# Performance work log

Hardware: AMD Instinct MI355X
Metric: run time of the kernel (lower is better)

Reference implementation:

```python
import jax, jax.numpy as jnp
import numpy as np

B, K, DIM, T_FRAMES = 4, 200, 256, 800

def _conv1d_same(x, w, b):
    # x: [B, K, Cin], w: [3, Cin, Cout] (WIO), 'same' padding over token axis
    y = jax.lax.conv_general_dilated(x, w, window_strides=(1,), padding='SAME',
                                     dimension_numbers=('NWC', 'WIO', 'NWC'))
    return y + b

def _swish_block(x, w1, b1, w2, b2):
    x = jax.nn.silu(x @ w1 + b1)
    return jax.nn.silu(x @ w2 + b2)

def setup_inputs() -> dict:
    key = jax.random.key(0)
    ks = jax.random.split(key, 10)
    def lin(k, fan_in, shape):
        return jax.random.normal(k, shape, dtype=jnp.float32) / np.sqrt(fan_in)
    inp = {
        'T': T_FRAMES,
        'durations': jax.random.uniform(ks[0], (B, K), dtype=jnp.float32) * 4.0,
        'features': jax.random.normal(ks[1], (B, K, DIM), dtype=jnp.float32),
        'conv1_w': lin(ks[2], 3 * DIM, (3, DIM, 8)),
        'conv1_b': jnp.zeros((8,), jnp.float32),
        'conv2_w': lin(ks[3], 3 * DIM, (3, DIM, 8)),
        'conv2_b': jnp.zeros((8,), jnp.float32),
        'sw1_w1': lin(ks[4], 10, (10, 16)), 'sw1_b1': jnp.zeros((16,), jnp.float32),
        'sw1_w2': lin(ks[5], 16, (16, 16)), 'sw1_b2': jnp.zeros((16,), jnp.float32),
        'sw2_w1': lin(ks[6], 10, (10, 2)), 'sw2_b1': jnp.zeros((2,), jnp.float32),
        'sw2_w2': lin(ks[7], 2, (2, 2)), 'sw2_b2': jnp.zeros((2,), jnp.float32),
        'p1_w': lin(ks[8], 2, (2, 1)), 'p1_b': jnp.zeros((1,), jnp.float32),
        'p2_w': lin(ks[9], 16, (16, DIM)), 'p2_b': jnp.zeros((DIM,), jnp.float32),
    }
    return inp

def reference(T, durations, features, conv1_w, conv1_b, conv2_w, conv2_b,
              sw1_w1, sw1_b1, sw1_w2, sw1_b2, sw2_w1, sw2_b1, sw2_w2, sw2_b2,
              p1_w, p1_b, p2_w, p2_b):
    # Conv + SiLU token feature extraction: [B, K, 8]
    left = jax.nn.silu(_conv1d_same(features, conv1_w, conv1_b))
    right = jax.nn.silu(_conv1d_same(features, conv2_w, conv2_b))
    # Token boundary grids S, E: [B, T, K]
    token_end = jnp.cumsum(durations, axis=1)          # [B, K]
    token_start = token_end - durations                # [B, K]
    t = jnp.arange(T, dtype=features.dtype)            # frame index grid
    S = t[None, :, None] - token_start[:, None, :]     # [B, T, K]
    E = token_end[:, None, :] - t[None, :, None]       # [B, T, K]
    Bn, Tn, Kn = S.shape
    # Concat (S, E, conv_feats) -> [B, T, K, 10]
    xleft = jnp.concatenate([S[..., None], E[..., None],
                             jnp.broadcast_to(left[:, None], (Bn, Tn, Kn, 8))], axis=-1)
    xright = jnp.concatenate([S[..., None], E[..., None],
                              jnp.broadcast_to(right[:, None], (Bn, Tn, Kn, 8))], axis=-1)
    C = _swish_block(xleft, sw1_w1, sw1_b1, sw1_w2, sw1_b2)      # [B, T, K, 16]
    r = _swish_block(xright, sw2_w1, sw2_b1, sw2_w2, sw2_b2)     # [B, T, K, 2]
    logits = (r @ p1_w + p1_b)[..., 0]                           # [B, T, K]
    W = jax.nn.softmax(logits, axis=-1)                          # attention over tokens
    # Upsampled output: weighted token features + projected auxiliary context
    O = jnp.einsum('btk,bkd->btd', W, features)
    A = jnp.einsum('btk,btkp->btp', W, C)                        # [B, T, 16]
    return O + (A @ p2_w + p2_b)
```

## Files before the change

kernel.cpp:

```cpp
#include <hip/hip_runtime.h>
#include <math.h>

#define B_   4
#define K_   200
#define DIM_ 256
#define T_   800

#define S_UP 68

__device__ __forceinline__ float silu_f(float x) {
    return x / (1.0f + __expf(-x));
}

__global__ __launch_bounds__(256) void prep_kernel(
        const float* __restrict__ dur,
        const float* __restrict__ feats,
        const float* __restrict__ c1w, const float* __restrict__ c1b,
        const float* __restrict__ c2w, const float* __restrict__ c2b,
        const float* __restrict__ sw1_w1, const float* __restrict__ sw1_b1,
        const float* __restrict__ sw2_w1, const float* __restrict__ sw2_b1,
        float* __restrict__ cw) {
    const int b = blockIdx.y, k0 = blockIdx.x * 4;
    const int tid = threadIdx.x, w = tid >> 6, l = tid & 63;

    __shared__ float wT[16][772];
    __shared__ float red[64][S_UP];
    __shared__ float sSc[K_], sEc[K_];
    __shared__ float sfeat[4][16];

    for (int i = tid; i < 3 * DIM_ * 8; i += 256) {
        int tc = i >> 3, o = i & 7;
        wT[o][tc]     = c1w[i];
        wT[8 + o][tc] = c2w[i];
    }
    if (tid < 64) {
        float4 dv = make_float4(0.f, 0.f, 0.f, 0.f);
        if (tid < 50) dv = *(const float4*)&dur[b * K_ + tid * 4];
        float s0 = dv.x, s1 = s0 + dv.y, s2 = s1 + dv.z, s3 = s2 + dv.w;
        float sc = s3;
#pragma unroll
        for (int off = 1; off < 64; off <<= 1) {
            float v = __shfl_up(sc, off);
            if (tid >= off) sc += v;
        }
        float excl = sc - s3;
        if (tid < 50) {
            *(float4*)&sSc[tid * 4] = make_float4(excl, excl + s0, excl + s1, excl + s2);
            *(float4*)&sEc[tid * 4] = make_float4(excl + s0, excl + s1, excl + s2, excl + s3);
        }
    }
    __syncthreads();

    {
        const int k = k0 + w;
        const float4* f4 = (const float4*)feats;
        float4 fv[3];
#pragma unroll
        for (int tap = 0; tap < 3; ++tap) {
            int kk = k - 1 + tap;
            bool valid = (kk >= 0 && kk < K_);
            int kc = valid ? kk : 0;
            float4 v = f4[(size_t)(b * K_ + kc) * 64 + l];
            fv[tap] = valid ? v : make_float4(0.f, 0.f, 0.f, 0.f);
        }
        float acc[16];
#pragma unroll
        for (int oc = 0; oc < 16; ++oc) acc[oc] = 0.f;
#pragma unroll
        for (int tap = 0; tap < 3; ++tap) {
#pragma unroll
            for (int oc = 0; oc < 16; ++oc) {
                float4 wv = *(const float4*)&wT[oc][tap * DIM_ + 4 * l];
                acc[oc] += fv[tap].x * wv.x + fv[tap].y * wv.y
                         + fv[tap].z * wv.z + fv[tap].w * wv.w;
            }
        }
#pragma unroll
        for (int oc = 0; oc < 16; ++oc) red[w * 16 + oc][l] = acc[oc];
    }
    __syncthreads();
    {
        const int rwv = tid >> 6, oc = (tid >> 2) & 15, rq = tid & 3;
        const float* base = &red[rwv * 16 + oc][rq * 16];
        float4 b0 = *(const float4*)&base[0];
        float4 b1 = *(const float4*)&base[4];
        float4 b2 = *(const float4*)&base[8];
        float4 b3 = *(const float4*)&base[12];
        float s = b0.x + b0.y + b0.z + b0.w + b1.x + b1.y + b1.z + b1.w
                + b2.x + b2.y + b2.z + b2.w + b3.x + b3.y + b3.z + b3.w;
        s += __shfl_down(s, 1);
        s += __shfl_down(s, 2);
        if (rq == 0) {
            float bias = (oc < 8) ? c1b[oc] : c2b[oc & 7];
            sfeat[rwv][oc] = silu_f(s + bias);
        }
    }
    __syncthreads();

    if (tid < 64) {
        const int j = tid >> 2, klc = tid & 3, kk = k0 + klc;
        float st = sSc[kk], en = sEc[kk];
        float a = sw1_b1[j] - st * sw1_w1[j] + en * sw1_w1[16 + j];
#pragma unroll
        for (int i = 0; i < 8; ++i) a += sfeat[klc][i] * sw1_w1[(2 + i) * 16 + j];
        cw[(b * 18 + 2 + j) * K_ + kk] = a;
    } else if (tid < 72) {
        const int idx = tid - 64, which = idx >> 2, klc = idx & 3, kk = k0 + klc;
        float st = sSc[kk], en = sEc[kk];
        float a = sw2_b1[which] - st * sw2_w1[which] + en * sw2_w1[2 + which];
#pragma unroll
        for (int i = 0; i < 8; ++i) a += sfeat[klc][8 + i] * sw2_w1[(2 + i) * 2 + which];
        cw[(b * 18 + which) * K_ + kk] = a;
    }
}

__global__ __launch_bounds__(256, 3) void main_kernel(
        const float* __restrict__ feats,
        const float* __restrict__ cw,
        const float* __restrict__ sw1_w1, const float* __restrict__ sw1_w2,
        const float* __restrict__ sw1_b2,
        const float* __restrict__ sw2_w1, const float* __restrict__ sw2_w2,
        const float* __restrict__ sw2_b2,
        const float* __restrict__ p1_w,   const float* __restrict__ p1_b,
        const float* __restrict__ p2_w,   const float* __restrict__ p2_b,
        float* __restrict__ out) {
    const int t0 = blockIdx.x * 4, b = blockIdx.y;
    const int tid = threadIdx.x, w = tid >> 6, l = tid & 63;
    const int t = t0 + w;

    __shared__ alignas(16) float upool[128 * S_UP];
    __shared__ alignas(16) float W4[K_][4];
    __shared__ alignas(16) float At[16][4];
    __shared__ float lw2T[16][16];
    __shared__ float lb2s[16];

    lw2T[tid & 15][tid >> 4] = sw1_w2[tid];
    if (tid < 16) lb2s[tid] = sw1_b2[tid];

    const float* cbg = cw + b * 18 * K_;
    int kc[4];
#pragma unroll
    for (int i = 0; i < 4; ++i) { int k = l + 64 * i; kc[i] = (k < K_) ? k : (K_ - 1); }
    float Bv[4][16];
#pragma unroll
    for (int j = 0; j < 16; ++j)
#pragma unroll
        for (int i = 0; i < 4; ++i) Bv[i][j] = cbg[(2 + j) * K_ + kc[i]];
    float c0[4], c1[4];
#pragma unroll
    for (int i = 0; i < 4; ++i) { c0[i] = cbg[kc[i]]; c1[i] = cbg[K_ + kc[i]]; }

    __syncthreads();

    const float tf = (float)t;
    const float a0 = sw2_w1[0] - sw2_w1[2], a1 = sw2_w1[1] - sw2_w1[3];
    const float rw20 = sw2_w2[0], rw21 = sw2_w2[1], rw22 = sw2_w2[2], rw23 = sw2_w2[3];
    const float rb20 = sw2_b2[0], rb21 = sw2_b2[1];
    const float p10 = p1_w[0], p11 = p1_w[1], p1b0 = p1_b[0];

    float lg[4];
#pragma unroll
    for (int i = 0; i < 4; ++i) {
        float h0 = silu_f(fmaf(a0, tf, c0[i]));
        float h1 = silu_f(fmaf(a1, tf, c1[i]));
        float g0 = silu_f(rb20 + h0 * rw20 + h1 * rw22);
        float g1 = silu_f(rb21 + h0 * rw21 + h1 * rw23);
        lg[i] = (l + 64 * i < K_) ? (g0 * p10 + g1 * p11 + p1b0) : -1e30f;
    }
    float m = fmaxf(fmaxf(lg[0], lg[1]), fmaxf(lg[2], lg[3]));
#pragma unroll
    for (int off = 32; off > 0; off >>= 1) m = fmaxf(m, __shfl_xor(m, off));
    float e0 = __expf(lg[0] - m), e1 = __expf(lg[1] - m);
    float e2 = __expf(lg[2] - m), e3 = __expf(lg[3] - m);
    float ssum = e0 + e1 + e2 + e3;
#pragma unroll
    for (int off = 32; off > 0; off >>= 1) ssum += __shfl_xor(ssum, off);
    float inv = 1.0f / ssum;
    float wgt[4] = { e0 * inv, e1 * inv, e2 * inv, e3 * inv };
#pragma unroll
    for (int i = 0; i < 4; ++i) { int k = l + 64 * i; if (k < K_) W4[k][w] = wgt[i]; }

    const int kb = w * 50;
    const float4* fB4 = (const float4*)(feats + (size_t)b * K_ * DIM_);
    float4 pf[8];
#pragma unroll
    for (int q = 0; q < 8; ++q) pf[q] = fB4[(size_t)(kb + q) * 64 + l];

    float ajt[16];
#pragma unroll
    for (int j = 0; j < 16; ++j) ajt[j] = (sw1_w1[j] - sw1_w1[16 + j]) * tf;
    float hmat[4][16];
#pragma unroll
    for (int j = 0; j < 16; ++j)
#pragma unroll
        for (int i = 0; i < 4; ++i) hmat[i][j] = silu_f(ajt[j] + Bv[i][j]);
    float acc[16];
#pragma unroll
    for (int j = 0; j < 16; ++j) {
        float4 w0 = *(const float4*)&lw2T[j][0];
        float4 w1v = *(const float4*)&lw2T[j][4];
        float4 w2v = *(const float4*)&lw2T[j][8];
        float4 w3v = *(const float4*)&lw2T[j][12];
        float bj = lb2s[j];
        float s = 0.f;
#pragma unroll
        for (int i = 0; i < 4; ++i) {
            float c = bj
                + hmat[i][0]  * w0.x  + hmat[i][1]  * w0.y  + hmat[i][2]  * w0.z  + hmat[i][3]  * w0.w
                + hmat[i][4]  * w1v.x + hmat[i][5]  * w1v.y + hmat[i][6]  * w1v.z + hmat[i][7]  * w1v.w
                + hmat[i][8]  * w2v.x + hmat[i][9]  * w2v.y + hmat[i][10] * w2v.z + hmat[i][11] * w2v.w
                + hmat[i][12] * w3v.x + hmat[i][13] * w3v.y + hmat[i][14] * w3v.z + hmat[i][15] * w3v.w;
            s += wgt[i] * silu_f(c);
        }
        acc[j] = s;
    }
#pragma unroll
    for (int j = 0; j < 16; ++j) upool[(w * 16 + j) * S_UP + l] = acc[j];

    __syncthreads();

    {
        const int rwv = tid >> 6, rj = (tid >> 2) & 15, rq = tid & 3;
        const float* base = &upool[(rwv * 16 + rj) * S_UP + rq * 16];
        float4 b0 = *(const float4*)&base[0];
        float4 b1 = *(const float4*)&base[4];
        float4 b2 = *(const float4*)&base[8];
        float4 b3 = *(const float4*)&base[12];
        float s = b0.x + b0.y + b0.z + b0.w + b1.x + b1.y + b1.z + b1.w
                + b2.x + b2.y + b2.z + b2.w + b3.x + b3.y + b3.z + b3.w;
        s += __shfl_down(s, 1);
        s += __shfl_down(s, 2);
        if (rq == 0) At[rj][rwv] = s;
    }

    {
        float4 po[4];
#pragma unroll
        for (int f = 0; f < 4; ++f) po[f] = make_float4(0.f, 0.f, 0.f, 0.f);
#pragma unroll
        for (int kk = 0; kk < 8; ++kk) {
            float4 wv = *(const float4*)&W4[kb + kk][0];
            float4 fv = pf[kk];
            po[0].x += wv.x * fv.x; po[0].y += wv.x * fv.y; po[0].z += wv.x * fv.z; po[0].w += wv.x * fv.w;
            po[1].x += wv.y * fv.x; po[1].y += wv.y * fv.y; po[1].z += wv.y * fv.z; po[1].w += wv.y * fv.w;
            po[2].x += wv.z * fv.x; po[2].y += wv.z * fv.y; po[2].z += wv.z * fv.z; po[2].w += wv.z * fv.w;
            po[3].x += wv.w * fv.x; po[3].y += wv.w * fv.y; po[3].z += wv.w * fv.z; po[3].w += wv.w * fv.w;
        }
#pragma unroll 6
        for (int kk = 8; kk < 50; ++kk) {
            float4 wv = *(const float4*)&W4[kb + kk][0];
            float4 fv = fB4[(size_t)(kb + kk) * 64 + l];
            po[0].x += wv.x * fv.x; po[0].y += wv.x * fv.y; po[0].z += wv.x * fv.z; po[0].w += wv.x * fv.w;
            po[1].x += wv.y * fv.x; po[1].y += wv.y * fv.y; po[1].z += wv.y * fv.z; po[1].w += wv.y * fv.w;
            po[2].x += wv.z * fv.x; po[2].y += wv.z * fv.y; po[2].z += wv.z * fv.z; po[2].w += wv.z * fv.w;
            po[3].x += wv.w * fv.x; po[3].y += wv.w * fv.y; po[3].z += wv.w * fv.z; po[3].w += wv.w * fv.w;
        }
#pragma unroll
        for (int f = 0; f < 4; ++f) {
            upool[(64 + w * 16 + f * 4 + 0) * S_UP + l] = po[f].x;
            upool[(64 + w * 16 + f * 4 + 1) * S_UP + l] = po[f].y;
            upool[(64 + w * 16 + f * 4 + 2) * S_UP + l] = po[f].z;
            upool[(64 + w * 16 + f * 4 + 3) * S_UP + l] = po[f].w;
        }
    }
    __syncthreads();

    {
        const int d = tid, l0 = d >> 2, q = d & 3;
        float v0 = 0.f, v1 = 0.f, v2 = 0.f, v3 = 0.f;
#pragma unroll
        for (int ww = 0; ww < 4; ++ww) {
            v0 += upool[(64 + ww * 16 + 0 * 4 + q) * S_UP + l0];
            v1 += upool[(64 + ww * 16 + 1 * 4 + q) * S_UP + l0];
            v2 += upool[(64 + ww * 16 + 2 * 4 + q) * S_UP + l0];
            v3 += upool[(64 + ww * 16 + 3 * 4 + q) * S_UP + l0];
        }
        float ab = p2_b[d];
        v0 += ab; v1 += ab; v2 += ab; v3 += ab;
#pragma unroll
        for (int p = 0; p < 16; ++p) {
            float pw = p2_w[p * DIM_ + d];
            float4 av = *(const float4*)&At[p][0];
            v0 += av.x * pw; v1 += av.y * pw; v2 += av.z * pw; v3 += av.w * pw;
        }
        float* op = out + ((size_t)b * T_ + t0) * DIM_ + d;
        op[0 * DIM_] = v0;
        op[1 * DIM_] = v1;
        op[2 * DIM_] = v2;
        op[3 * DIM_] = v3;
    }
}

extern "C" void kernel_launch(void* const* d_in, const int* in_sizes, int n_in,
                              void* d_out, int out_size, void* d_ws, size_t ws_size,
                              hipStream_t stream) {
    const float* durations = (const float*)d_in[1];
    const float* features  = (const float*)d_in[2];
    const float* conv1_w   = (const float*)d_in[3];
    const float* conv1_b   = (const float*)d_in[4];
    const float* conv2_w   = (const float*)d_in[5];
    const float* conv2_b   = (const float*)d_in[6];
    const float* sw1_w1    = (const float*)d_in[7];
    const float* sw1_b1    = (const float*)d_in[8];
    const float* sw1_w2    = (const float*)d_in[9];
    const float* sw1_b2    = (const float*)d_in[10];
    const float* sw2_w1    = (const float*)d_in[11];
    const float* sw2_b1    = (const float*)d_in[12];
    const float* sw2_w2    = (const float*)d_in[13];
    const float* sw2_b2    = (const float*)d_in[14];
    const float* p1_w      = (const float*)d_in[15];
    const float* p1_b      = (const float*)d_in[16];
    const float* p2_w      = (const float*)d_in[17];
    const float* p2_b      = (const float*)d_in[18];
    float* out = (float*)d_out;

    float* cw = (float*)d_ws;

    prep_kernel<<<dim3(50, B_), 256, 0, stream>>>(
        durations, features, conv1_w, conv1_b, conv2_w, conv2_b,
        sw1_w1, sw1_b1, sw2_w1, sw2_b1, cw);
    main_kernel<<<dim3(T_ / 4, B_), 256, 0, stream>>>(
        features, cw,
        sw1_w1, sw1_w2, sw1_b2,
        sw2_w1, sw2_w2, sw2_b2,
        p1_w, p1_b, p2_w, p2_b, out);
}
```

Measured before the change: 130.2 us.

## Restructure main kernel to 8 frames per 512-thread block with contiguous token tiles

```diff
diff --git a/kernel.cpp b/kernel.cpp
--- a/kernel.cpp
+++ b/kernel.cpp
@@ -7,9 +7,15 @@
 #define T_   800
 
 #define S_UP 68
+#define S_O  66
+#define KP_  204
 
 __device__ __forceinline__ float silu_f(float x) {
     return x / (1.0f + __expf(-x));
+}
+__device__ __forceinline__ void fma4(float4& a, float s, const float4& v) {
+    a.x = fmaf(s, v.x, a.x); a.y = fmaf(s, v.y, a.y);
+    a.z = fmaf(s, v.z, a.z); a.w = fmaf(s, v.w, a.w);
 }
 
 __global__ __launch_bounds__(256) void prep_kernel(
@@ -114,7 +120,7 @@
     }
 }
 
-__global__ __launch_bounds__(256, 3) void main_kernel(
+__global__ __launch_bounds__(512, 4) void main_kernel(
         const float* __restrict__ feats,
         const float* __restrict__ cw,
         const float* __restrict__ sw1_w1, const float* __restrict__ sw1_w2,
@@ -124,48 +130,48 @@
         const float* __restrict__ p1_w,   const float* __restrict__ p1_b,
         const float* __restrict__ p2_w,   const float* __restrict__ p2_b,
         float* __restrict__ out) {
-    const int t0 = blockIdx.x * 4, b = blockIdx.y;
+    const int t0 = blockIdx.x * 8, b = blockIdx.y;
     const int tid = threadIdx.x, w = tid >> 6, l = tid & 63;
-    const int t = t0 + w;
-
-    __shared__ alignas(16) float upool[128 * S_UP];
-    __shared__ alignas(16) float W4[K_][4];
-    __shared__ alignas(16) float At[16][4];
-    __shared__ float lw2T[16][16];
-    __shared__ float lb2s[16];
-
-    lw2T[tid & 15][tid >> 4] = sw1_w2[tid];
+    const float tf = (float)(t0 + w);
+
+    __shared__ alignas(16) float upool[128 * S_O];
+    __shared__ alignas(16) float W8[8][KP_];
+    __shared__ alignas(16) float At[16][8];
+    __shared__ alignas(16) float lw2R[256];
+    __shared__ alignas(16) float lb2s[16];
+
+    if (tid < 256) lw2R[tid] = sw1_w2[tid];
     if (tid < 16) lb2s[tid] = sw1_b2[tid];
 
+    const int  kbase = (l < 50) ? 4 * l : 196;
+    const bool kv    = (l < 50);
     const float* cbg = cw + b * 18 * K_;
-    int kc[4];
-#pragma unroll
-    for (int i = 0; i < 4; ++i) { int k = l + 64 * i; kc[i] = (k < K_) ? k : (K_ - 1); }
-    float Bv[4][16];
-#pragma unroll
-    for (int j = 0; j < 16; ++j)
-#pragma unroll
-        for (int i = 0; i < 4; ++i) Bv[i][j] = cbg[(2 + j) * K_ + kc[i]];
-    float c0[4], c1[4];
-#pragma unroll
-    for (int i = 0; i < 4; ++i) { c0[i] = cbg[kc[i]]; c1[i] = cbg[K_ + kc[i]]; }
-
-    __syncthreads();
-
-    const float tf = (float)t;
+
+    float4 c0v = *(const float4*)&cbg[kbase];
+    float4 c1v = *(const float4*)&cbg[K_ + kbase];
+    float4 Bcur[4], Bnxt[4];
+#pragma unroll
+    for (int j = 0; j < 4; ++j) Bcur[j] = *(const float4*)&cbg[(2 + j) * K_ + kbase];
+
+    __syncthreads();
+
     const float a0 = sw2_w1[0] - sw2_w1[2], a1 = sw2_w1[1] - sw2_w1[3];
     const float rw20 = sw2_w2[0], rw21 = sw2_w2[1], rw22 = sw2_w2[2], rw23 = sw2_w2[3];
     const float rb20 = sw2_b2[0], rb21 = sw2_b2[1];
     const float p10 = p1_w[0], p11 = p1_w[1], p1b0 = p1_b[0];
 
     float lg[4];
-#pragma unroll
-    for (int i = 0; i < 4; ++i) {
-        float h0 = silu_f(fmaf(a0, tf, c0[i]));
-        float h1 = silu_f(fmaf(a1, tf, c1[i]));
-        float g0 = silu_f(rb20 + h0 * rw20 + h1 * rw22);
-        float g1 = silu_f(rb21 + h0 * rw21 + h1 * rw23);
-        lg[i] = (l + 64 * i < K_) ? (g0 * p10 + g1 * p11 + p1b0) : -1e30f;
+    {
+        float c0a[4] = { c0v.x, c0v.y, c0v.z, c0v.w };
+        float c1a[4] = { c1v.x, c1v.y, c1v.z, c1v.w };
+#pragma unroll
+        for (int i = 0; i < 4; ++i) {
+            float h0 = silu_f(fmaf(a0, tf, c0a[i]));
+            float h1 = silu_f(fmaf(a1, tf, c1a[i]));
+            float g0 = silu_f(rb20 + h0 * rw20 + h1 * rw22);
+            float g1 = silu_f(rb21 + h0 * rw21 + h1 * rw23);
+            lg[i] = kv ? (g0 * p10 + g1 * p11 + p1b0) : -1e30f;
+        }
     }
     float m = fmaxf(fmaxf(lg[0], lg[1]), fmaxf(lg[2], lg[3]));
 #pragma unroll
@@ -177,51 +183,65 @@
     for (int off = 32; off > 0; off >>= 1) ssum += __shfl_xor(ssum, off);
     float inv = 1.0f / ssum;
     float wgt[4] = { e0 * inv, e1 * inv, e2 * inv, e3 * inv };
-#pragma unroll
-    for (int i = 0; i < 4; ++i) { int k = l + 64 * i; if (k < K_) W4[k][w] = wgt[i]; }
-
-    const int kb = w * 50;
+    if (kv) *(float4*)&W8[w][kbase] = make_float4(wgt[0], wgt[1], wgt[2], wgt[3]);
+
+    const int kb = 25 * w;
     const float4* fB4 = (const float4*)(feats + (size_t)b * K_ * DIM_);
-    float4 pf[8];
-#pragma unroll
-    for (int q = 0; q < 8; ++q) pf[q] = fB4[(size_t)(kb + q) * 64 + l];
-
-    float ajt[16];
-#pragma unroll
-    for (int j = 0; j < 16; ++j) ajt[j] = (sw1_w1[j] - sw1_w1[16 + j]) * tf;
-    float hmat[4][16];
-#pragma unroll
-    for (int j = 0; j < 16; ++j)
-#pragma unroll
-        for (int i = 0; i < 4; ++i) hmat[i][j] = silu_f(ajt[j] + Bv[i][j]);
-    float acc[16];
-#pragma unroll
-    for (int j = 0; j < 16; ++j) {
-        float4 w0 = *(const float4*)&lw2T[j][0];
-        float4 w1v = *(const float4*)&lw2T[j][4];
-        float4 w2v = *(const float4*)&lw2T[j][8];
-        float4 w3v = *(const float4*)&lw2T[j][12];
-        float bj = lb2s[j];
-        float s = 0.f;
-#pragma unroll
-        for (int i = 0; i < 4; ++i) {
-            float c = bj
-                + hmat[i][0]  * w0.x  + hmat[i][1]  * w0.y  + hmat[i][2]  * w0.z  + hmat[i][3]  * w0.w
-                + hmat[i][4]  * w1v.x + hmat[i][5]  * w1v.y + hmat[i][6]  * w1v.z + hmat[i][7]  * w1v.w
-                + hmat[i][8]  * w2v.x + hmat[i][9]  * w2v.y + hmat[i][10] * w2v.z + hmat[i][11] * w2v.w
-                + hmat[i][12] * w3v.x + hmat[i][13] * w3v.y + hmat[i][14] * w3v.z + hmat[i][15] * w3v.w;
-            s += wgt[i] * silu_f(c);
-        }
-        acc[j] = s;
-    }
-#pragma unroll
-    for (int j = 0; j < 16; ++j) upool[(w * 16 + j) * S_UP + l] = acc[j];
-
-    __syncthreads();
-
+    float4 pf0 = fB4[(size_t)kb * 64 + l];
+    float4 pf1 = fB4[(size_t)(kb + 1) * 64 + l];
+
+    float4 cacc[4][4];
+#pragma unroll
+    for (int i = 0; i < 4; ++i)
+#pragma unroll
+        for (int q = 0; q < 4; ++q) cacc[i][q] = make_float4(0.f, 0.f, 0.f, 0.f);
+
+#pragma unroll
+    for (int grp = 0; grp < 4; ++grp) {
+        if (grp < 3) {
+#pragma unroll
+            for (int j = 0; j < 4; ++j)
+                Bnxt[j] = *(const float4*)&cbg[(2 + grp * 4 + 4 + j) * K_ + kbase];
+        }
+#pragma unroll
+        for (int j = 0; j < 4; ++j) {
+            const int jj = grp * 4 + j;
+            float aj = (sw1_w1[jj] - sw1_w1[16 + jj]) * tf;
+            float h0 = silu_f(aj + Bcur[j].x);
+            float h1 = silu_f(aj + Bcur[j].y);
+            float h2 = silu_f(aj + Bcur[j].z);
+            float h3 = silu_f(aj + Bcur[j].w);
+#pragma unroll
+            for (int q = 0; q < 4; ++q) {
+                float4 wv = *(const float4*)&lw2R[jj * 16 + 4 * q];
+                fma4(cacc[0][q], h0, wv);
+                fma4(cacc[1][q], h1, wv);
+                fma4(cacc[2][q], h2, wv);
+                fma4(cacc[3][q], h3, wv);
+            }
+        }
+#pragma unroll
+        for (int j = 0; j < 4; ++j) Bcur[j] = Bnxt[j];
+    }
+#pragma unroll
+    for (int q = 0; q < 4; ++q) {
+        float4 bb = *(const float4*)&lb2s[4 * q];
+        float sx = wgt[0] * silu_f(cacc[0][q].x + bb.x) + wgt[1] * silu_f(cacc[1][q].x + bb.x)
+                 + wgt[2] * silu_f(cacc[2][q].x + bb.x) + wgt[3] * silu_f(cacc[3][q].x + bb.x);
+        float sy = wgt[0] * silu_f(cacc[0][q].y + bb.y) + wgt[1] * silu_f(cacc[1][q].y + bb.y)
+                 + wgt[2] * silu_f(cacc[2][q].y + bb.y) + wgt[3] * silu_f(cacc[3][q].y + bb.y);
+        float sz = wgt[0] * silu_f(cacc[0][q].z + bb.z) + wgt[1] * silu_f(cacc[1][q].z + bb.z)
+                 + wgt[2] * silu_f(cacc[2][q].z + bb.z) + wgt[3] * silu_f(cacc[3][q].z + bb.z);
+        float sw = wgt[0] * silu_f(cacc[0][q].w + bb.w) + wgt[1] * silu_f(cacc[1][q].w + bb.w)
+                 + wgt[2] * silu_f(cacc[2][q].w + bb.w) + wgt[3] * silu_f(cacc[3][q].w + bb.w);
+        upool[(w * 16 + 4 * q + 0) * S_O + l] = sx;
+        upool[(w * 16 + 4 * q + 1) * S_O + l] = sy;
+        upool[(w * 16 + 4 * q + 2) * S_O + l] = sz;
+        upool[(w * 16 + 4 * q + 3) * S_O + l] = sw;
+    }
     {
-        const int rwv = tid >> 6, rj = (tid >> 2) & 15, rq = tid & 3;
-        const float* base = &upool[(rwv * 16 + rj) * S_UP + rq * 16];
+        const int rj = (l >> 2) & 15, rq = l & 3;
+        const float* base = &upool[(w * 16 + rj) * S_O + rq * 16];
         float4 b0 = *(const float4*)&base[0];
         float4 b1 = *(const float4*)&base[4];
         float4 b2 = *(const float4*)&base[8];
@@ -230,64 +250,57 @@
                 + b2.x + b2.y + b2.z + b2.w + b3.x + b3.y + b3.z + b3.w;
         s += __shfl_down(s, 1);
         s += __shfl_down(s, 2);
-        if (rq == 0) At[rj][rwv] = s;
-    }
-
-    {
+        if (rq == 0) At[rj][w] = s;
+    }
+    __syncthreads();
+
+    const int d = tid & 255, f0 = tid >> 8;
+    const int l0 = d >> 2, qq = d & 3;
+
+#pragma unroll
+    for (int half = 0; half < 2; ++half) {
         float4 po[4];
 #pragma unroll
         for (int f = 0; f < 4; ++f) po[f] = make_float4(0.f, 0.f, 0.f, 0.f);
-#pragma unroll
-        for (int kk = 0; kk < 8; ++kk) {
-            float4 wv = *(const float4*)&W4[kb + kk][0];
-            float4 fv = pf[kk];
-            po[0].x += wv.x * fv.x; po[0].y += wv.x * fv.y; po[0].z += wv.x * fv.z; po[0].w += wv.x * fv.w;
-            po[1].x += wv.y * fv.x; po[1].y += wv.y * fv.y; po[1].z += wv.y * fv.z; po[1].w += wv.y * fv.w;
-            po[2].x += wv.z * fv.x; po[2].y += wv.z * fv.y; po[2].z += wv.z * fv.z; po[2].w += wv.z * fv.w;
-            po[3].x += wv.w * fv.x; po[3].y += wv.w * fv.y; po[3].z += wv.w * fv.z; po[3].w += wv.w * fv.w;
-        }
-#pragma unroll 6
-        for (int kk = 8; kk < 50; ++kk) {
-            float4 wv = *(const float4*)&W4[kb + kk][0];
-            float4 fv = fB4[(size_t)(kb + kk) * 64 + l];
-            po[0].x += wv.x * fv.x; po[0].y += wv.x * fv.y; po[0].z += wv.x * fv.z; po[0].w += wv.x * fv.w;
-            po[1].x += wv.y * fv.x; po[1].y += wv.y * fv.y; po[1].z += wv.y * fv.z; po[1].w += wv.y * fv.w;
-            po[2].x += wv.z * fv.x; po[2].y += wv.z * fv.y; po[2].z += wv.z * fv.z; po[2].w += wv.z * fv.w;
-            po[3].x += wv.w * fv.x; po[3].y += wv.w * fv.y; po[3].z += wv.w * fv.z; po[3].w += wv.w * fv.w;
+        const float* Wr0 = W8[half * 4 + 0];
+        const float* Wr1 = W8[half * 4 + 1];
+        const float* Wr2 = W8[half * 4 + 2];
+        const float* Wr3 = W8[half * 4 + 3];
+#pragma unroll 5
+        for (int kk = 0; kk < 25; ++kk) {
+            const int k = kb + kk;
+            float4 fv;
+            if (half == 0 && kk == 0)      fv = pf0;
+            else if (half == 0 && kk == 1) fv = pf1;
+            else                           fv = fB4[(size_t)k * 64 + l];
+            float w0 = Wr0[k], w1 = Wr1[k], w2 = Wr2[k], w3 = Wr3[k];
+            fma4(po[0], w0, fv);
+            fma4(po[1], w1, fv);
+            fma4(po[2], w2, fv);
+            fma4(po[3], w3, fv);
         }
 #pragma unroll
         for (int f = 0; f < 4; ++f) {
-            upool[(64 + w * 16 + f * 4 + 0) * S_UP + l] = po[f].x;
-            upool[(64 + w * 16 + f * 4 + 1) * S_UP + l] = po[f].y;
-            upool[(64 + w * 16 + f * 4 + 2) * S_UP + l] = po[f].z;
-            upool[(64 + w * 16 + f * 4 + 3) * S_UP + l] = po[f].w;
-        }
-    }
-    __syncthreads();
-
-    {
-        const int d = tid, l0 = d >> 2, q = d & 3;
-        float v0 = 0.f, v1 = 0.f, v2 = 0.f, v3 = 0.f;
-#pragma unroll
-        for (int ww = 0; ww < 4; ++ww) {
-            v0 += upool[(64 + ww * 16 + 0 * 4 + q) * S_UP + l0];
-            v1 += upool[(64 + ww * 16 + 1 * 4 + q) * S_UP + l0];
-            v2 += upool[(64 + ww * 16 + 2 * 4 + q) * S_UP + l0];
-            v3 += upool[(64 + ww * 16 + 3 * 4 + q) * S_UP + l0];
-        }
-        float ab = p2_b[d];
-        v0 += ab; v1 += ab; v2 += ab; v3 += ab;
-#pragma unroll
-        for (int p = 0; p < 16; ++p) {
-            float pw = p2_w[p * DIM_ + d];
-            float4 av = *(const float4*)&At[p][0];
-            v0 += av.x * pw; v1 += av.y * pw; v2 += av.z * pw; v3 += av.w * pw;
-        }
-        float* op = out + ((size_t)b * T_ + t0) * DIM_ + d;
-        op[0 * DIM_] = v0;
-        op[1 * DIM_] = v1;
-        op[2 * DIM_] = v2;
-        op[3 * DIM_] = v3;
+            upool[(w * 16 + f * 4 + 0) * S_O + l] = po[f].x;
+            upool[(w * 16 + f * 4 + 1) * S_O + l] = po[f].y;
+            upool[(w * 16 + f * 4 + 2) * S_O + l] = po[f].z;
+            upool[(w * 16 + f * 4 + 3) * S_O + l] = po[f].w;
+        }
+        __syncthreads();
+
+#pragma unroll
+        for (int ffi = 0; ffi < 2; ++ffi) {
+            const int fr = f0 + 2 * ffi;
+            float v = p2_b[d];
+#pragma unroll
+            for (int ww = 0; ww < 8; ++ww)
+                v += upool[(ww * 16 + fr * 4 + qq) * S_O + l0];
+#pragma unroll
+            for (int p = 0; p < 16; ++p)
+                v += At[p][half * 4 + fr] * p2_w[p * DIM_ + d];
+            out[((size_t)b * T_ + t0 + half * 4 + fr) * DIM_ + d] = v;
+        }
+        if (half == 0) __syncthreads();
     }
 }
 
@@ -319,7 +332,7 @@
     prep_kernel<<<dim3(50, B_), 256, 0, stream>>>(
         durations, features, conv1_w, conv1_b, conv2_w, conv2_b,
         sw1_w1, sw1_b1, sw2_w1, sw2_b1, cw);
-    main_kernel<<<dim3(T_ / 4, B_), 256, 0, stream>>>(
+    main_kernel<<<dim3(T_ / 8, B_), 512, 0, stream>>>(
         features, cw,
         sw1_w1, sw1_w2, sw1_b2,
         sw2_w1, sw2_w2, sw2_b2,
```

Measured after the change: 131.8 us. About the same (+1.2%).
